# Optimization experiments

Measured on AMD Instinct MI355X. Metric: run time of the kernel, lower is better.

## Reference

```python
import jax, jax.numpy as jnp
import numpy as np

N_NODES = 50000
N_EDGES = 800000
IN_DIM = 256
HID = 256
NUM_LAYERS = 2


def _sage(xin, src, dst, inv_deg, W_l, b_l, W_r):
    # PyG SAGEConv (mean aggr): lin_l(mean of src features scattered to dst) + lin_r(x)
    agg = jax.ops.segment_sum(xin[src], dst, num_segments=xin.shape[0]) * inv_deg
    return agg @ W_l + b_l + xin @ W_r


def _mgdsgu(x, src, dst, inv_deg, h, Wx_l, bx_l, Wx_r, Wh_l, bh_l, Wh_r, Wb1, bb1, Wb2, bb2):
    # hid->hid conv order: 0=sage_hidden, 1=sage_single_h, 2=sage_update_h, 3=sage_candidate_h
    # in ->hid conv order: 0=sage_single_x, 1=sage_update_x, 2=sage_candidate_x
    h_N = _sage(h, src, dst, inv_deg, Wh_l[0], bh_l[0], Wh_r[0])
    # predict_missing_info: r = zeros so r_v = beta; gamma is computed in the
    # original but multiplied by zero -> no effect (omitted).
    beta = jnp.tanh(h @ Wb1 + bb1 + h_N @ Wb2 + bb2)
    m = h + beta - h_N
    h_N = h_N + m  # == h + beta, kept as written for clarity
    r = jax.nn.sigmoid(_sage(x, src, dst, inv_deg, Wx_l[0], bx_l[0], Wx_r[0])
                       + _sage(h_N, src, dst, inv_deg, Wh_l[1], bh_l[1], Wh_r[1]))
    z = jax.nn.sigmoid(_sage(x, src, dst, inv_deg, Wx_l[1], bx_l[1], Wx_r[1])
                       + _sage(h_N, src, dst, inv_deg, Wh_l[2], bh_l[2], Wh_r[2]))
    h_tilde = jnp.tanh(_sage(x, src, dst, inv_deg, Wx_l[2], bx_l[2], Wx_r[2])
                       + _sage(r * h_N, src, dst, inv_deg, Wh_l[3], bh_l[3], Wh_r[3]))
    return (1.0 - z) * h_N + z * h_tilde


def setup_inputs() -> dict:
    key = jax.random.key(0)
    ks = jax.random.split(key, 12)
    sx = 1.0 / np.sqrt(IN_DIM)
    sh = 1.0 / np.sqrt(HID)
    inp = {
        "x": jax.random.normal(ks[0], (N_NODES, IN_DIM), dtype=jnp.float32),
        "edge_index": jax.random.randint(ks[1], (2, N_EDGES), 0, N_NODES, dtype=jnp.int64),
        "Wx_l": jax.random.normal(ks[2], (3, IN_DIM, HID), dtype=jnp.float32) * sx,
        "bx_l": jnp.zeros((3, HID), dtype=jnp.float32),
        "Wx_r": jax.random.normal(ks[3], (3, IN_DIM, HID), dtype=jnp.float32) * sx,
        "Wh_l": jax.random.normal(ks[4], (4, HID, HID), dtype=jnp.float32) * sh,
        "bh_l": jnp.zeros((4, HID), dtype=jnp.float32),
        "Wh_r": jax.random.normal(ks[5], (4, HID, HID), dtype=jnp.float32) * sh,
        "Wb1": jax.random.normal(ks[6], (HID, HID), dtype=jnp.float32) * sh,
        "bb1": jnp.zeros((HID,), dtype=jnp.float32),
        "Wb2": jax.random.normal(ks[7], (HID, HID), dtype=jnp.float32) * sh,
        "bb2": jnp.zeros((HID,), dtype=jnp.float32),
        "We1": jax.random.normal(ks[8], (2 * HID, HID), dtype=jnp.float32) * (1.0 / np.sqrt(2 * HID)),
        "be1": jnp.zeros((HID,), dtype=jnp.float32),
        "We2": jax.random.normal(ks[9], (HID, 1), dtype=jnp.float32) * sh,
        "be2": jnp.zeros((1,), dtype=jnp.float32),
    }
    return inp


def reference(x, edge_index, Wx_l, bx_l, Wx_r, Wh_l, bh_l, Wh_r,
              Wb1, bb1, Wb2, bb2, We1, be1, We2, be2):
    src, dst = edge_index[0], edge_index[1]
    deg = jax.ops.segment_sum(jnp.ones((src.shape[0],), dtype=x.dtype), dst,
                              num_segments=x.shape[0])
    inv_deg = (1.0 / jnp.maximum(deg, 1.0))[:, None]  # [N, 1]

    h = jnp.zeros((x.shape[0], HID), dtype=x.dtype)
    for _ in range(NUM_LAYERS):
        h = _mgdsgu(x, src, dst, inv_deg, h, Wx_l, bx_l, Wx_r,
                    Wh_l, bh_l, Wh_r, Wb1, bb1, Wb2, bb2)

    # edge embeddings: concat(src emb, dst emb) -> MLP -> sigmoid
    edge_emb = jnp.concatenate([h[src], h[dst]], axis=1)  # [E, 2H]
    hidden = jax.nn.relu(edge_emb @ We1 + be1)
    preds = jax.nn.sigmoid(hidden @ We2 + be2)  # [E, 1]
    return (preds, h)
```

## Files before the change

kernel.cpp:

```cpp
#include <hip/hip_runtime.h>
#include <math.h>

#define HID 256
#define LROW 40

typedef __bf16 bf16x8 __attribute__((ext_vector_type(8)));
typedef float  f32x4  __attribute__((ext_vector_type(4)));
typedef unsigned short us8 __attribute__((ext_vector_type(8)));

__device__ __forceinline__ float sigmoidf_(float x){ return 1.0f/(1.0f + __expf(-x)); }
__device__ __forceinline__ unsigned short f2b(float f){
  __bf16 b = (__bf16)f; return __builtin_bit_cast(unsigned short, b);
}
__device__ __forceinline__ float b2f(unsigned short u){
  return (float)__builtin_bit_cast(__bf16, u);
}

__device__ __forceinline__ int edge_src(const int* ei, int e, int is64){
  return is64 ? ei[2*e] : ei[e];
}
__device__ __forceinline__ int edge_dst(const int* ei, int e, int E, int is64){
  return is64 ? ei[2*(E+e)] : ei[E+e];
}

__global__ void detect_kernel(const int* __restrict__ ei, int* __restrict__ flag){
  __shared__ int any;
  if (threadIdx.x == 0) any = 0;
  __syncthreads();
  if (ei[2*threadIdx.x + 1] != 0) atomicOr(&any, 1);
  __syncthreads();
  if (threadIdx.x == 0) *flag = any ? 0 : 1;
}

__global__ void count_kernel(const int* __restrict__ ei, const int* __restrict__ flag,
                             int* __restrict__ deg_i, int E){
  int e = blockIdx.x*blockDim.x + threadIdx.x;
  if (e >= E) return;
  int is64 = *flag;
  atomicAdd(&deg_i[edge_dst(ei,e,E,is64)], 1);
}

__global__ __launch_bounds__(1024) void scan_kernel(const int* __restrict__ deg_i,
  int* __restrict__ row_ptr, float* __restrict__ inv_deg, int N)
{
  __shared__ int wsum[16];
  __shared__ int carry_s;
  int tid = threadIdx.x, lane = tid & 63, wid = tid >> 6;
  if (tid == 0) carry_s = 0;
  __syncthreads();
  for (int base = 0; base < N; base += 1024){
    int i = base + tid;
    int v = (i < N) ? deg_i[i] : 0;
    int s = v;
    #pragma unroll
    for (int off = 1; off < 64; off <<= 1){
      int t = __shfl_up(s, off, 64);
      if (lane >= off) s += t;
    }
    if (lane == 63) wsum[wid] = s;
    __syncthreads();
    if (tid == 0){
      int run = 0;
      for (int w2 = 0; w2 < 16; ++w2){ int t = wsum[w2]; wsum[w2] = run; run += t; }
    }
    __syncthreads();
    int excl = carry_s + wsum[wid] + s - v;
    if (i < N){
      row_ptr[i] = excl;
      inv_deg[i] = 1.0f / fmaxf((float)v, 1.0f);
    }
    __syncthreads();
    if (tid == 1023) carry_s = excl + v;
    __syncthreads();
  }
  if (threadIdx.x == 0) row_ptr[N] = carry_s;
}

__global__ void fill_kernel(const int* __restrict__ ei, const int* __restrict__ flag,
                            const int* __restrict__ row_ptr, int* __restrict__ cursor,
                            int* __restrict__ col_src, int E){
  int e = blockIdx.x*blockDim.x + threadIdx.x;
  if (e >= E) return;
  int is64 = *flag;
  int d = edge_dst(ei,e,E,is64);
  int pos = atomicAdd(&cursor[d], 1);
  col_src[row_ptr[d] + pos] = edge_src(ei,e,is64);
}

__global__ __launch_bounds__(256) void conv_kernel(const float* __restrict__ in,
                                                   unsigned short* __restrict__ out, int n4){
  int i = blockIdx.x*256 + threadIdx.x;
  if (i >= n4) return;
  float4 v = *(const float4*)&in[(size_t)i*4];
  ushort4 o; o.x=f2b(v.x); o.y=f2b(v.y); o.z=f2b(v.z); o.w=f2b(v.w);
  *(ushort4*)&out[(size_t)i*4] = o;
}

__global__ __launch_bounds__(256) void wconv_kernel(
  const float* __restrict__ Wx_l, const float* __restrict__ Wx_r,
  const float* __restrict__ Wh_l, const float* __restrict__ Wh_r,
  const float* __restrict__ Wb1,  const float* __restrict__ Wb2,
  const float* __restrict__ We1,  unsigned short* __restrict__ Wt)
{
  int widx = blockIdx.x;
  int n = blockIdx.y;
  int k = threadIdx.x;
  const float* src;
  if      (widx < 3)  src = Wx_l + widx*65536;
  else if (widx < 6)  src = Wx_r + (widx-3)*65536;
  else if (widx < 10) src = Wh_l + (widx-6)*65536;
  else if (widx < 14) src = Wh_r + (widx-10)*65536;
  else if (widx == 14) src = Wb1;
  else if (widx == 15) src = Wb2;
  else                src = We1 + (widx-16)*65536;
  Wt[(size_t)widx*65536 + n*256 + k] = f2b(src[k*256 + n]);
}

__global__ __launch_bounds__(256) void comp_kernel(
  const float* __restrict__ A, const float* __restrict__ B,
  const float* __restrict__ add, unsigned short* __restrict__ dst)
{
  __shared__ float col[256];
  int n = blockIdx.x, k = threadIdx.x;
  col[k] = B[k*256 + n];
  __syncthreads();
  float s = add ? add[k*256 + n] : 0.f;
  #pragma unroll 8
  for (int j = 0; j < 256; ++j) s = fmaf(A[k*256 + j], col[j], s);
  dst[n*256 + k] = f2b(s);
}

__global__ __launch_bounds__(256) void aggregate_b_kernel(
    const unsigned short* __restrict__ X, unsigned short* __restrict__ out,
    const int* __restrict__ row_ptr, const int* __restrict__ col_src,
    const float* __restrict__ inv_deg, int N)
{
  int v = blockIdx.x*4 + (threadIdx.x >> 6);
  int lane = threadIdx.x & 63;
  if (v >= N) return;
  int beg = row_ptr[v], end = row_ptr[v+1];
  float a0=0.f, a1=0.f, a2=0.f, a3=0.f;
  int e = beg;
  for (; e + 8 <= end; e += 8){
    int sidx[8];
    #pragma unroll
    for (int t = 0; t < 8; ++t) sidx[t] = col_src[e + t];
    #pragma unroll
    for (int t = 0; t < 8; ++t){
      ushort4 u = *(const ushort4*)&X[(size_t)sidx[t]*HID + lane*4];
      a0 += b2f(u.x); a1 += b2f(u.y); a2 += b2f(u.z); a3 += b2f(u.w);
    }
  }
  for (; e < end; ++e){
    int s0 = col_src[e];
    ushort4 u = *(const ushort4*)&X[(size_t)s0*HID + lane*4];
    a0 += b2f(u.x); a1 += b2f(u.y); a2 += b2f(u.z); a3 += b2f(u.w);
  }
  float w = inv_deg[v];
  ushort4 o; o.x=f2b(a0*w); o.y=f2b(a1*w); o.z=f2b(a2*w); o.w=f2b(a3*w);
  *(ushort4*)&out[(size_t)v*HID + lane*4] = o;
}

__global__ __launch_bounds__(256) void rowprep_kernel(
  const float* __restrict__ bh_l, const float* __restrict__ bb1, const float* __restrict__ bb2,
  const float* __restrict__ Wb2, const float* __restrict__ Wh_l, const float* __restrict__ Wh_r,
  float* __restrict__ brow, float* __restrict__ hrow,
  float* __restrict__ rowL1, float* __restrict__ rowR1,
  float* __restrict__ rowL2, float* __restrict__ rowR2)
{
  __shared__ float sh[256];
  __shared__ float sh2[256];
  int j = threadIdx.x;
  sh[j] = bh_l[j];
  __syncthreads();
  float acc = bb1[j] + bb2[j];
  for (int k = 0; k < 256; ++k) acc = fmaf(sh[k], Wb2[k*256 + j], acc);
  float hr = tanhf(acc);
  brow[j] = acc;
  hrow[j] = hr; sh2[j] = hr;
  __syncthreads();
  const float* Whl1 = Wh_l + 65536;  const float* Whr1 = Wh_r + 65536;
  const float* Whl2 = Wh_l + 131072; const float* Whr2 = Wh_r + 131072;
  float a1=0.f, b1=0.f, a2=0.f, b2v=0.f;
  for (int k = 0; k < 256; ++k){
    float hv = sh2[k];
    a1  = fmaf(hv, Whl1[k*256+j], a1);
    b1  = fmaf(hv, Whr1[k*256+j], b1);
    a2  = fmaf(hv, Whl2[k*256+j], a2);
    b2v = fmaf(hv, Whr2[k*256+j], b2v);
  }
  rowL1[j] = a1; rowR1[j] = b1 + bh_l[256 + j];
  rowL2[j] = a2; rowR2[j] = b2v + bh_l[512 + j];
}

struct GJob {
  const unsigned short *A0,*W0,*A1,*W1,*A2,*W2,*A3,*W3;
  const float *bias,*bias2,*Z,*HN;
  const float *rowA,*rowB,*mulrow,*mulmat;
  const int* deg;
  float* outF; unsigned short* outB;
  int hn_bcast;
};

template<int MODE>
__global__ __launch_bounds__(512) void mgemm3_kernel(GJob j0, GJob j1, int M)
{
  __shared__ unsigned short Al[128*LROW];
  __shared__ unsigned short Wl[256*LROW];
  const GJob& J = blockIdx.y ? j1 : j0;
  const int tid  = threadIdx.x;
  const int lane = tid & 63, w = tid >> 6;
  const int wr = w >> 2, wc = w & 3;
  const int lane15 = lane & 15, laneq = (lane >> 4) * 8;
  const int row0 = blockIdx.x * 128;

  f32x4 acc[4][4];
  #pragma unroll
  for (int m = 0; m < 4; ++m)
    #pragma unroll
    for (int n = 0; n < 4; ++n) acc[m][n] = (f32x4)0.f;

  const unsigned short* pa[4]; const unsigned short* pw[4];
  int np = 0;
  if (J.A0){ pa[np]=J.A0; pw[np]=J.W0; ++np; }
  if (J.A1){ pa[np]=J.A1; pw[np]=J.W1; ++np; }
  if (J.A2){ pa[np]=J.A2; pw[np]=J.W2; ++np; }
  if (J.A3){ pa[np]=J.A3; pw[np]=J.W3; ++np; }
  const int steps = np * 8;

  const int strow = tid >> 2;
  const int koff  = (tid & 3) * 8;
  const int garow = (row0 + strow > M-1) ? (M-1) : (row0 + strow);
  const size_t abase  = (size_t)garow*HID + koff;
  const size_t wbase0 = (size_t)strow*HID + koff;
  const size_t wbase1 = (size_t)(strow + 128)*HID + koff;
  const int asidx  = strow*LROW + koff;
  const int wsidx0 = strow*LROW + koff;
  const int wsidx1 = (strow + 128)*LROW + koff;

  uint4 Ar0,Wr0a,Wr0b, Ar1,Wr1a,Wr1b;
  auto loadR = [&](int sp, uint4& a, uint4& wa, uint4& wb){
    const unsigned short* Ap = pa[sp >> 3];
    const unsigned short* Wp = pw[sp >> 3];
    const int k0 = (sp & 7) * 32;
    a  = *(const uint4*)(Ap + abase  + k0);
    wa = *(const uint4*)(Wp + wbase0 + k0);
    wb = *(const uint4*)(Wp + wbase1 + k0);
  };
  auto compute = [&](){
    bf16x8 af[4], bfr[4];
    #pragma unroll
    for (int m = 0; m < 4; ++m)
      af[m] = *(const bf16x8*)&Al[(wr*64 + m*16 + lane15)*LROW + laneq];
    #pragma unroll
    for (int n = 0; n < 4; ++n)
      bfr[n] = *(const bf16x8*)&Wl[(wc*64 + n*16 + lane15)*LROW + laneq];
    #pragma unroll
    for (int m = 0; m < 4; ++m)
      #pragma unroll
      for (int n = 0; n < 4; ++n)
        acc[m][n] = __builtin_amdgcn_mfma_f32_16x16x32_bf16(af[m], bfr[n], acc[m][n], 0, 0, 0);
  };

  loadR(0, Ar0,Wr0a,Wr0b);
  loadR(1, Ar1,Wr1a,Wr1b);
  for (int s = 0; s < steps; s += 2){
    __syncthreads();
    *(uint4*)&Al[asidx]  = Ar0;
    *(uint4*)&Wl[wsidx0] = Wr0a;
    *(uint4*)&Wl[wsidx1] = Wr0b;
    __syncthreads();
    if (s + 2 < steps) loadR(s+2, Ar0,Wr0a,Wr0b);
    compute();
    __syncthreads();
    *(uint4*)&Al[asidx]  = Ar1;
    *(uint4*)&Wl[wsidx0] = Wr1a;
    *(uint4*)&Wl[wsidx1] = Wr1b;
    __syncthreads();
    if (s + 3 < steps) loadR(s+3, Ar1,Wr1a,Wr1b);
    compute();
  }

  #pragma unroll
  for (int n = 0; n < 4; ++n){
    int gc = wc*64 + n*16 + lane15;
    float badd = 0.f;
    if (J.bias)  badd += J.bias[gc];
    if (J.bias2) badd += J.bias2[gc];
    float rA = 0.f, rB = 0.f, mr = 1.f, hnb = 0.f;
    if (MODE == 1){
      if (J.rowA){ rA = J.rowA[gc]; rB = J.rowB[gc]; }
      if (J.mulrow) mr = J.mulrow[gc];
    }
    if (MODE == 3 && J.hn_bcast) hnb = J.HN[gc];
    #pragma unroll
    for (int m = 0; m < 4; ++m){
      int rbse = row0 + wr*64 + m*16 + ((lane >> 4) << 2);
      #pragma unroll
      for (int r = 0; r < 4; ++r){
        int gr = rbse + r;
        if (gr >= M) continue;
        size_t idx = (size_t)gr*HID + gc;
        float p = acc[m][n][r] + badd;
        float v;
        if (MODE == 0) v = p;
        else if (MODE == 1){
          float g = (J.rowA && J.deg) ? ((J.deg[gr] > 0) ? 1.f : 0.f) : 0.f;
          v = sigmoidf_(p + g*rA + rB);
          if (J.mulrow) v *= mr;
          if (J.mulmat) v *= J.mulmat[idx];
        } else if (MODE == 2){
          v = J.HN[idx] + tanhf(p);
        } else {
          float z  = J.Z[idx];
          float hv = J.hn_bcast ? hnb : J.HN[idx];
          v = (1.f - z)*hv + z*tanhf(p);
        }
        if (J.outF) J.outF[idx] = v;
        if (J.outB) J.outB[idx] = f2b(v);
      }
    }
  }
}

__global__ __launch_bounds__(256) void edge_pred_kernel(
  const unsigned short* __restrict__ P, const unsigned short* __restrict__ Q,
  const int* __restrict__ ei, const int* __restrict__ flag,
  const float* __restrict__ We2, const float* __restrict__ be2,
  float* __restrict__ preds, int E)
{
  int wid = blockIdx.x*8 + (threadIdx.x >> 5);
  int l = threadIdx.x & 31;
  if (wid >= E) return;
  int is64 = *flag;
  int s = edge_src(ei, wid, is64);
  int d = edge_dst(ei, wid, E, is64);
  us8 p8 = *(const us8*)&P[(size_t)s*HID + l*8];
  us8 q8 = *(const us8*)&Q[(size_t)d*HID + l*8];
  float4 w0 = *(const float4*)&We2[l*8];
  float4 w1 = *(const float4*)&We2[l*8 + 4];
  float part = 0.f;
  #pragma unroll
  for (int j = 0; j < 4; ++j)
    part = fmaf(fmaxf(b2f(p8[j]) + b2f(q8[j]), 0.f), (&w0.x)[j], part);
  #pragma unroll
  for (int j = 0; j < 4; ++j)
    part = fmaf(fmaxf(b2f(p8[4+j]) + b2f(q8[4+j]), 0.f), (&w1.x)[j], part);
  #pragma unroll
  for (int off = 16; off > 0; off >>= 1) part += __shfl_down(part, off, 32);
  if (l == 0) preds[wid] = sigmoidf_(part + be2[0]);
}

typedef const unsigned short* cus;
typedef const float* cf;

template<int MODE>
static void launch_f(const GJob& a, const GJob* b, int M, hipStream_t s){
  dim3 g((M + 127)/128, b ? 2 : 1), blk(512);
  mgemm3_kernel<MODE><<<g, blk, 0, s>>>(a, b ? *b : a, M);
}

extern "C" void kernel_launch(void* const* d_in, const int* in_sizes, int n_in,
                              void* d_out, int out_size, void* d_ws, size_t ws_size,
                              hipStream_t stream)
{
  const float* x    = (const float*)d_in[0];
  const int*   ei   = (const int*)  d_in[1];
  const float* Wx_l = (const float*)d_in[2];
  const float* bx_l = (const float*)d_in[3];
  const float* Wx_r = (const float*)d_in[4];
  const float* Wh_l = (const float*)d_in[5];
  const float* bh_l = (const float*)d_in[6];
  const float* Wh_r = (const float*)d_in[7];
  const float* Wb1  = (const float*)d_in[8];
  const float* bb1  = (const float*)d_in[9];
  const float* Wb2  = (const float*)d_in[10];
  const float* bb2  = (const float*)d_in[11];
  const float* We1  = (const float*)d_in[12];
  const float* be1  = (const float*)d_in[13];
  const float* We2  = (const float*)d_in[14];
  const float* be2  = (const float*)d_in[15];

  const int N = in_sizes[0] / HID;
  const int E = in_sizes[1] / 2;
  cf NUL = nullptr; cus NUB = nullptr; const int* NULI = nullptr;

  size_t off = 0;
  auto alloc = [&](size_t bytes) -> void* {
    void* p = (char*)d_ws + off;
    off += (bytes + 255) & ~(size_t)255;
    return p;
  };
  int*   deg_i   = (int*)  alloc((size_t)N*4);
  int*   cursor  = (int*)  alloc((size_t)N*4);
  int*   row_ptr = (int*)  alloc(((size_t)N+1)*4);
  int*   col_src = (int*)  alloc((size_t)E*4);
  float* inv_deg = (float*)alloc((size_t)N*4);
  int*   flag    = (int*)  alloc(256);
  float* brow    = (float*)alloc(1024);
  float* hrow    = (float*)alloc(1024);
  float* rowL1   = (float*)alloc(1024);
  float* rowR1   = (float*)alloc(1024);
  float* rowL2   = (float*)alloc(1024);
  float* rowR2   = (float*)alloc(1024);
  unsigned short* Wt = (unsigned short*)alloc((size_t)18*65536*2);
  float* F0 = (float*)alloc((size_t)N*HID*4);
  float* F1 = (float*)alloc((size_t)N*HID*4);
  unsigned short* b0 = (unsigned short*)alloc((size_t)N*HID*2);
  unsigned short* b1 = (unsigned short*)alloc((size_t)N*HID*2);
  unsigned short* b2 = (unsigned short*)alloc((size_t)N*HID*2);
  unsigned short* b3 = (unsigned short*)alloc((size_t)N*HID*2);
  unsigned short* b4 = (unsigned short*)alloc((size_t)N*HID*2);

  float* preds = (float*)d_out;
  float* H     = preds + E;

  auto WT = [&](int i) -> cus { return Wt + (size_t)i*65536; };
  const float* bx0 = bx_l;  const float* bx1 = bx_l + 256; const float* bx2 = bx_l + 512;
  const float* bh1 = bh_l + 256;
  const float* bh2 = bh_l + 512; const float* bh3 = bh_l + 768;

  const int eb  = (E + 255)/256;
  const int nb4 = (N + 3)/4;
  const int n4b = (N*64 + 255)/256;

  auto mkjob = [&](cus A0,cus W0,cus A1,cus W1,cus A2,cus W2,cus A3,cus W3,
                   cf bias, cf bias2, cf Z, cf HN, int hnb,
                   cf rA, cf rB, cf mr, cf mm, const int* dg,
                   float* oF, unsigned short* oB) -> GJob {
    GJob g;
    g.A0=A0; g.W0=W0; g.A1=A1; g.W1=W1; g.A2=A2; g.W2=W2; g.A3=A3; g.W3=W3;
    g.bias=bias; g.bias2=bias2; g.Z=Z; g.HN=HN; g.hn_bcast=hnb;
    g.rowA=rA; g.rowB=rB; g.mulrow=mr; g.mulmat=mm; g.deg=dg;
    g.outF=oF; g.outB=oB;
    return g;
  };

  hipMemsetAsync(deg_i, 0, (size_t)N*4, stream);
  hipMemsetAsync(cursor, 0, (size_t)N*4, stream);
  detect_kernel<<<1,256,0,stream>>>(ei, flag);
  count_kernel<<<eb,256,0,stream>>>(ei, flag, deg_i, E);
  scan_kernel<<<1,1024,0,stream>>>(deg_i, row_ptr, inv_deg, N);
  fill_kernel<<<eb,256,0,stream>>>(ei, flag, row_ptr, cursor, col_src, E);

  conv_kernel<<<n4b,256,0,stream>>>(x, b0, N*64);
  wconv_kernel<<<dim3(18,256),256,0,stream>>>(Wx_l, Wx_r, Wh_l, Wh_r, Wb1, Wb2, We1, Wt);
  comp_kernel<<<256,256,0,stream>>>(Wh_l, Wb2, nullptr, (unsigned short*)WT(14));
  comp_kernel<<<256,256,0,stream>>>(Wh_r, Wb2, Wb1,     (unsigned short*)WT(15));
  rowprep_kernel<<<1,256,0,stream>>>(bh_l, bb1, bb2, Wb2, Wh_l, Wh_r,
                                     brow, hrow, rowL1, rowR1, rowL2, rowR2);

  aggregate_b_kernel<<<nb4,256,0,stream>>>(b0, b1, row_ptr, col_src, inv_deg, N);
  {
    GJob jt = mkjob(b1,WT(0), b0,WT(3), NUB,NUB, NUB,NUB, bx0,NUL, NUL,NUL,0,
                    rowL1,rowR1, hrow,NUL, deg_i, nullptr, b2);
    GJob jz = mkjob(b1,WT(1), b0,WT(4), NUB,NUB, NUB,NUB, bx1,NUL, NUL,NUL,0,
                    rowL2,rowR2, NUL,NUL, deg_i, F0, nullptr);
    launch_f<1>(jt, &jz, N, stream);
  }
  aggregate_b_kernel<<<nb4,256,0,stream>>>(b2, b3, row_ptr, col_src, inv_deg, N);
  {
    GJob jh = mkjob(b3,WT(9), b2,WT(13), b1,WT(2), b0,WT(5), bx2,bh3, F0,hrow,1,
                    NUL,NUL, NUL,NUL, NULI, F0, b4);
    launch_f<3>(jh, nullptr, N, stream);
  }

  aggregate_b_kernel<<<nb4,256,0,stream>>>(b4, b2, row_ptr, col_src, inv_deg, N);
  {
    GJob jn = mkjob(b2,WT(14), b4,WT(15), NUB,NUB, NUB,NUB, brow,NUL, NUL,F0,0,
                    NUL,NUL, NUL,NUL, NULI, F1, b3);
    launch_f<2>(jn, nullptr, N, stream);
  }
  aggregate_b_kernel<<<nb4,256,0,stream>>>(b3, b2, row_ptr, col_src, inv_deg, N);
  {
    GJob jt = mkjob(b2,WT(7), b3,WT(11), b1,WT(0), b0,WT(3), bx0,bh1, NUL,NUL,0,
                    NUL,NUL, NUL,F1, NULI, nullptr, b4);
    GJob jz = mkjob(b2,WT(8), b3,WT(12), b1,WT(1), b0,WT(4), bx1,bh2, NUL,NUL,0,
                    NUL,NUL, NUL,NUL, NULI, F0, nullptr);
    launch_f<1>(jt, &jz, N, stream);
  }
  aggregate_b_kernel<<<nb4,256,0,stream>>>(b4, b2, row_ptr, col_src, inv_deg, N);
  {
    GJob jh = mkjob(b2,WT(9), b4,WT(13), b1,WT(2), b0,WT(5), bx2,bh3, F0,F1,0,
                    NUL,NUL, NUL,NUL, NULI, H, b3);
    launch_f<3>(jh, nullptr, N, stream);
  }

  {
    GJob jp = mkjob(b3,WT(16), NUB,NUB, NUB,NUB, NUB,NUB, be1,NUL, NUL,NUL,0,
                    NUL,NUL, NUL,NUL, NULI, nullptr, b2);
    GJob jq = mkjob(b3,WT(17), NUB,NUB, NUB,NUB, NUB,NUB, NUL,NUL, NUL,NUL,0,
                    NUL,NUL, NUL,NUL, NULI, nullptr, b4);
    launch_f<0>(jp, &jq, N, stream);
  }
  edge_pred_kernel<<<(E+7)/8,256,0,stream>>>(b2, b4, ei, flag, We2, be2, preds, E);
}
```

Measured before the change: 1.160 ms.

## Precompute shared x-projections once and reuse across both GRU layers

The x-side SAGE projections (x and aggregated x against the three input weight sets) are identical in both layers. They are now computed once in a single three-job GEMM launch, stored as bf16/fp32 tensors, and added as epilogue inputs in later GEMMs, which cuts the K dimension of the layer-2 and candidate GEMMs from four operand pairs to two. Layer-1 gating moves to a separate elementwise kernel, and the GEMM tile is halved to 64 rows to give more blocks. The cost is extra intermediate traffic and bf16 rounding of the stored projections, which adds some precision risk.

Result: slower. 1.207 ms (+4.0%).

```diff
diff --git a/kernel.cpp b/kernel.cpp
--- a/kernel.cpp
+++ b/kernel.cpp
@@ -193,30 +193,61 @@
   rowL2[j] = a2; rowR2[j] = b2v + bh_l[512 + j];
 }
 
+__global__ __launch_bounds__(256) void l1_elem_kernel(
+  const unsigned short* __restrict__ xc0, const unsigned short* __restrict__ xc1,
+  const int* __restrict__ deg_i, const float* __restrict__ hrow,
+  const float* __restrict__ rowL1, const float* __restrict__ rowR1,
+  const float* __restrict__ rowL2, const float* __restrict__ rowR2,
+  unsigned short* __restrict__ t1, float* __restrict__ z1, int N)
+{
+  int idx = blockIdx.x*256 + threadIdx.x;
+  if (idx >= N*64) return;
+  int v = idx >> 6, j4 = (idx & 63) * 4;
+  float g = deg_i[v] > 0 ? 1.f : 0.f;
+  ushort4 a = *(const ushort4*)&xc0[(size_t)idx*4];
+  ushort4 b = *(const ushort4*)&xc1[(size_t)idx*4];
+  float4 L1 = *(const float4*)&rowL1[j4];
+  float4 R1 = *(const float4*)&rowR1[j4];
+  float4 L2 = *(const float4*)&rowL2[j4];
+  float4 R2 = *(const float4*)&rowR2[j4];
+  float4 hr = *(const float4*)&hrow[j4];
+  ushort4 t; float4 z;
+  t.x = f2b(sigmoidf_(b2f(a.x) + g*L1.x + R1.x) * hr.x);
+  t.y = f2b(sigmoidf_(b2f(a.y) + g*L1.y + R1.y) * hr.y);
+  t.z = f2b(sigmoidf_(b2f(a.z) + g*L1.z + R1.z) * hr.z);
+  t.w = f2b(sigmoidf_(b2f(a.w) + g*L1.w + R1.w) * hr.w);
+  z.x = sigmoidf_(b2f(b.x) + g*L2.x + R2.x);
+  z.y = sigmoidf_(b2f(b.y) + g*L2.y + R2.y);
+  z.z = sigmoidf_(b2f(b.z) + g*L2.z + R2.z);
+  z.w = sigmoidf_(b2f(b.w) + g*L2.w + R2.w);
+  *(ushort4*)&t1[(size_t)idx*4] = t;
+  *(float4*)&z1[(size_t)idx*4] = z;
+}
+
 struct GJob {
   const unsigned short *A0,*W0,*A1,*W1,*A2,*W2,*A3,*W3;
   const float *bias,*bias2,*Z,*HN;
-  const float *rowA,*rowB,*mulrow,*mulmat;
-  const int* deg;
+  const float *mulmat,*Df;
+  const unsigned short *Db,*Zb;
   float* outF; unsigned short* outB;
   int hn_bcast;
 };
 
 template<int MODE>
-__global__ __launch_bounds__(512) void mgemm3_kernel(GJob j0, GJob j1, int M)
-{
-  __shared__ unsigned short Al[128*LROW];
+__global__ __launch_bounds__(512) void mgemm4_kernel(GJob j0, GJob j1, GJob j2, int M)
+{
+  __shared__ unsigned short Al[64*LROW];
   __shared__ unsigned short Wl[256*LROW];
-  const GJob& J = blockIdx.y ? j1 : j0;
+  const GJob& J = (blockIdx.y == 0) ? j0 : ((blockIdx.y == 1) ? j1 : j2);
   const int tid  = threadIdx.x;
   const int lane = tid & 63, w = tid >> 6;
   const int wr = w >> 2, wc = w & 3;
   const int lane15 = lane & 15, laneq = (lane >> 4) * 8;
-  const int row0 = blockIdx.x * 128;
-
-  f32x4 acc[4][4];
+  const int row0 = blockIdx.x * 64;
+
+  f32x4 acc[2][4];
   #pragma unroll
-  for (int m = 0; m < 4; ++m)
+  for (int m = 0; m < 2; ++m)
     #pragma unroll
     for (int n = 0; n < 4; ++n) acc[m][n] = (f32x4)0.f;
 
@@ -228,35 +259,35 @@
   if (J.A3){ pa[np]=J.A3; pw[np]=J.W3; ++np; }
   const int steps = np * 8;
 
-  const int strow = tid >> 2;
-  const int koff  = (tid & 3) * 8;
-  const int garow = (row0 + strow > M-1) ? (M-1) : (row0 + strow);
-  const size_t abase  = (size_t)garow*HID + koff;
-  const size_t wbase0 = (size_t)strow*HID + koff;
-  const size_t wbase1 = (size_t)(strow + 128)*HID + koff;
-  const int asidx  = strow*LROW + koff;
-  const int wsidx0 = strow*LROW + koff;
-  const int wsidx1 = (strow + 128)*LROW + koff;
-
-  uint4 Ar0,Wr0a,Wr0b, Ar1,Wr1a,Wr1b;
-  auto loadR = [&](int sp, uint4& a, uint4& wa, uint4& wb){
+  const int arow  = tid >> 3;
+  const int akoff = (tid & 7) * 4;
+  const int garow = (row0 + arow > M-1) ? (M-1) : (row0 + arow);
+  const size_t abase = (size_t)garow*HID + akoff;
+  const int asidx = arow*LROW + akoff;
+  const int wrow  = tid >> 1;
+  const int wkoff = (tid & 1) * 16;
+  const size_t wbase = (size_t)wrow*HID + wkoff;
+  const int wsidx = wrow*LROW + wkoff;
+
+  uint2 Ar0, Ar1; uint4 Wr0a, Wr0b, Wr1a, Wr1b;
+  auto loadR = [&](int sp, uint2& a, uint4& wa, uint4& wb){
     const unsigned short* Ap = pa[sp >> 3];
     const unsigned short* Wp = pw[sp >> 3];
     const int k0 = (sp & 7) * 32;
-    a  = *(const uint4*)(Ap + abase  + k0);
-    wa = *(const uint4*)(Wp + wbase0 + k0);
-    wb = *(const uint4*)(Wp + wbase1 + k0);
+    a  = *(const uint2*)(Ap + abase + k0);
+    wa = *(const uint4*)(Wp + wbase + k0);
+    wb = *(const uint4*)(Wp + wbase + k0 + 8);
   };
   auto compute = [&](){
-    bf16x8 af[4], bfr[4];
-    #pragma unroll
-    for (int m = 0; m < 4; ++m)
-      af[m] = *(const bf16x8*)&Al[(wr*64 + m*16 + lane15)*LROW + laneq];
+    bf16x8 af[2], bfr[4];
+    #pragma unroll
+    for (int m = 0; m < 2; ++m)
+      af[m] = *(const bf16x8*)&Al[(wr*32 + m*16 + lane15)*LROW + laneq];
     #pragma unroll
     for (int n = 0; n < 4; ++n)
       bfr[n] = *(const bf16x8*)&Wl[(wc*64 + n*16 + lane15)*LROW + laneq];
     #pragma unroll
-    for (int m = 0; m < 4; ++m)
+    for (int m = 0; m < 2; ++m)
       #pragma unroll
       for (int n = 0; n < 4; ++n)
         acc[m][n] = __builtin_amdgcn_mfma_f32_16x16x32_bf16(af[m], bfr[n], acc[m][n], 0, 0, 0);
@@ -266,16 +297,16 @@
   loadR(1, Ar1,Wr1a,Wr1b);
   for (int s = 0; s < steps; s += 2){
     __syncthreads();
-    *(uint4*)&Al[asidx]  = Ar0;
-    *(uint4*)&Wl[wsidx0] = Wr0a;
-    *(uint4*)&Wl[wsidx1] = Wr0b;
+    *(uint2*)&Al[asidx]    = Ar0;
+    *(uint4*)&Wl[wsidx]    = Wr0a;
+    *(uint4*)&Wl[wsidx+8]  = Wr0b;
     __syncthreads();
     if (s + 2 < steps) loadR(s+2, Ar0,Wr0a,Wr0b);
     compute();
     __syncthreads();
-    *(uint4*)&Al[asidx]  = Ar1;
-    *(uint4*)&Wl[wsidx0] = Wr1a;
-    *(uint4*)&Wl[wsidx1] = Wr1b;
+    *(uint2*)&Al[asidx]    = Ar1;
+    *(uint4*)&Wl[wsidx]    = Wr1a;
+    *(uint4*)&Wl[wsidx+8]  = Wr1b;
     __syncthreads();
     if (s + 3 < steps) loadR(s+3, Ar1,Wr1a,Wr1b);
     compute();
@@ -287,32 +318,28 @@
     float badd = 0.f;
     if (J.bias)  badd += J.bias[gc];
     if (J.bias2) badd += J.bias2[gc];
-    float rA = 0.f, rB = 0.f, mr = 1.f, hnb = 0.f;
-    if (MODE == 1){
-      if (J.rowA){ rA = J.rowA[gc]; rB = J.rowB[gc]; }
-      if (J.mulrow) mr = J.mulrow[gc];
-    }
+    float hnb = 0.f;
     if (MODE == 3 && J.hn_bcast) hnb = J.HN[gc];
     #pragma unroll
-    for (int m = 0; m < 4; ++m){
-      int rbse = row0 + wr*64 + m*16 + ((lane >> 4) << 2);
+    for (int m = 0; m < 2; ++m){
+      int rbse = row0 + wr*32 + m*16 + ((lane >> 4) << 2);
       #pragma unroll
       for (int r = 0; r < 4; ++r){
         int gr = rbse + r;
         if (gr >= M) continue;
         size_t idx = (size_t)gr*HID + gc;
         float p = acc[m][n][r] + badd;
+        if (J.Df) p += J.Df[idx];
+        if (J.Db) p += b2f(J.Db[idx]);
         float v;
         if (MODE == 0) v = p;
         else if (MODE == 1){
-          float g = (J.rowA && J.deg) ? ((J.deg[gr] > 0) ? 1.f : 0.f) : 0.f;
-          v = sigmoidf_(p + g*rA + rB);
-          if (J.mulrow) v *= mr;
+          v = sigmoidf_(p);
           if (J.mulmat) v *= J.mulmat[idx];
         } else if (MODE == 2){
           v = J.HN[idx] + tanhf(p);
         } else {
-          float z  = J.Z[idx];
+          float z  = J.Z ? J.Z[idx] : b2f(J.Zb[idx]);
           float hv = J.hn_bcast ? hnb : J.HN[idx];
           v = (1.f - z)*hv + z*tanhf(p);
         }
@@ -355,9 +382,9 @@
 typedef const float* cf;
 
 template<int MODE>
-static void launch_f(const GJob& a, const GJob* b, int M, hipStream_t s){
-  dim3 g((M + 127)/128, b ? 2 : 1), blk(512);
-  mgemm3_kernel<MODE><<<g, blk, 0, s>>>(a, b ? *b : a, M);
+static void launch_f(const GJob* j, int nj, int M, hipStream_t s){
+  dim3 g((M + 63)/64, nj), blk(512);
+  mgemm4_kernel<MODE><<<g, blk, 0, s>>>(j[0], nj > 1 ? j[1] : j[0], nj > 2 ? j[2] : j[0], M);
 }
 
 extern "C" void kernel_launch(void* const* d_in, const int* in_sizes, int n_in,
@@ -383,7 +410,7 @@
 
   const int N = in_sizes[0] / HID;
   const int E = in_sizes[1] / 2;
-  cf NUL = nullptr; cus NUB = nullptr; const int* NULI = nullptr;
+  cf NUL = nullptr; cus NUB = nullptr;
 
   size_t off = 0;
   auto alloc = [&](size_t bytes) -> void* {
@@ -410,7 +437,6 @@
   unsigned short* b1 = (unsigned short*)alloc((size_t)N*HID*2);
   unsigned short* b2 = (unsigned short*)alloc((size_t)N*HID*2);
   unsigned short* b3 = (unsigned short*)alloc((size_t)N*HID*2);
-  unsigned short* b4 = (unsigned short*)alloc((size_t)N*HID*2);
 
   float* preds = (float*)d_out;
   float* H     = preds + E;
@@ -424,14 +450,14 @@
   const int nb4 = (N + 3)/4;
   const int n4b = (N*64 + 255)/256;
 
-  auto mkjob = [&](cus A0,cus W0,cus A1,cus W1,cus A2,cus W2,cus A3,cus W3,
-                   cf bias, cf bias2, cf Z, cf HN, int hnb,
-                   cf rA, cf rB, cf mr, cf mm, const int* dg,
+  auto mkjob = [&](cus A0,cus W0,cus A1,cus W1,
+                   cf bias, cf Z, cf HN, int hnb,
+                   cf mulmat, cf Df, cus Db, cus Zb,
                    float* oF, unsigned short* oB) -> GJob {
     GJob g;
-    g.A0=A0; g.W0=W0; g.A1=A1; g.W1=W1; g.A2=A2; g.W2=W2; g.A3=A3; g.W3=W3;
-    g.bias=bias; g.bias2=bias2; g.Z=Z; g.HN=HN; g.hn_bcast=hnb;
-    g.rowA=rA; g.rowB=rB; g.mulrow=mr; g.mulmat=mm; g.deg=dg;
+    g.A0=A0; g.W0=W0; g.A1=A1; g.W1=W1; g.A2=NUB; g.W2=NUB; g.A3=NUB; g.W3=NUB;
+    g.bias=bias; g.bias2=NUL; g.Z=Z; g.HN=HN; g.hn_bcast=hnb;
+    g.mulmat=mulmat; g.Df=Df; g.Db=Db; g.Zb=Zb;
     g.outF=oF; g.outB=oB;
     return g;
   };
@@ -452,46 +478,47 @@
 
   aggregate_b_kernel<<<nb4,256,0,stream>>>(b0, b1, row_ptr, col_src, inv_deg, N);
   {
-    GJob jt = mkjob(b1,WT(0), b0,WT(3), NUB,NUB, NUB,NUB, bx0,NUL, NUL,NUL,0,
-                    rowL1,rowR1, hrow,NUL, deg_i, nullptr, b2);
-    GJob jz = mkjob(b1,WT(1), b0,WT(4), NUB,NUB, NUB,NUB, bx1,NUL, NUL,NUL,0,
-                    rowL2,rowR2, NUL,NUL, deg_i, F0, nullptr);
-    launch_f<1>(jt, &jz, N, stream);
-  }
-  aggregate_b_kernel<<<nb4,256,0,stream>>>(b2, b3, row_ptr, col_src, inv_deg, N);
+    GJob j[3] = {
+      mkjob(b1,WT(0), b0,WT(3), bx0, NUL,NUL,0, NUL,NUL,NUB,NUB, nullptr, b2),
+      mkjob(b1,WT(1), b0,WT(4), bx1, NUL,NUL,0, NUL,NUL,NUB,NUB, nullptr, b3),
+      mkjob(b1,WT(2), b0,WT(5), bx2, NUL,NUL,0, NUL,NUL,NUB,NUB, F0, nullptr)
+    };
+    launch_f<0>(j, 3, N, stream);
+  }
+
+  l1_elem_kernel<<<n4b,256,0,stream>>>(b2, b3, deg_i, hrow, rowL1, rowR1,
+                                       rowL2, rowR2, b0, F1, N);
+  aggregate_b_kernel<<<nb4,256,0,stream>>>(b0, b1, row_ptr, col_src, inv_deg, N);
   {
-    GJob jh = mkjob(b3,WT(9), b2,WT(13), b1,WT(2), b0,WT(5), bx2,bh3, F0,hrow,1,
-                    NUL,NUL, NUL,NUL, NULI, F0, b4);
-    launch_f<3>(jh, nullptr, N, stream);
-  }
-
-  aggregate_b_kernel<<<nb4,256,0,stream>>>(b4, b2, row_ptr, col_src, inv_deg, N);
+    GJob j = mkjob(b1,WT(9), b0,WT(13), bh3, F1,hrow,1, NUL,F0,NUB,NUB, F1, b0);
+    launch_f<3>(&j, 1, N, stream);
+  }
+
+  aggregate_b_kernel<<<nb4,256,0,stream>>>(b0, b1, row_ptr, col_src, inv_deg, N);
   {
-    GJob jn = mkjob(b2,WT(14), b4,WT(15), NUB,NUB, NUB,NUB, brow,NUL, NUL,F0,0,
-                    NUL,NUL, NUL,NUL, NULI, F1, b3);
-    launch_f<2>(jn, nullptr, N, stream);
-  }
-  aggregate_b_kernel<<<nb4,256,0,stream>>>(b3, b2, row_ptr, col_src, inv_deg, N);
+    GJob j = mkjob(b1,WT(14), b0,WT(15), brow, NUL,F1,0, NUL,NUL,NUB,NUB, F1, b0);
+    launch_f<2>(&j, 1, N, stream);
+  }
+  aggregate_b_kernel<<<nb4,256,0,stream>>>(b0, b1, row_ptr, col_src, inv_deg, N);
   {
-    GJob jt = mkjob(b2,WT(7), b3,WT(11), b1,WT(0), b0,WT(3), bx0,bh1, NUL,NUL,0,
-                    NUL,NUL, NUL,F1, NULI, nullptr, b4);
-    GJob jz = mkjob(b2,WT(8), b3,WT(12), b1,WT(1), b0,WT(4), bx1,bh2, NUL,NUL,0,
-                    NUL,NUL, NUL,NUL, NULI, F0, nullptr);
-    launch_f<1>(jt, &jz, N, stream);
-  }
-  aggregate_b_kernel<<<nb4,256,0,stream>>>(b4, b2, row_ptr, col_src, inv_deg, N);
+    GJob j[2] = {
+      mkjob(b1,WT(7), b0,WT(11), bh1, NUL,NUL,0, F1,NUL,b2,NUB, nullptr, b2),
+      mkjob(b1,WT(8), b0,WT(12), bh2, NUL,NUL,0, NUL,NUL,b3,NUB, nullptr, b3)
+    };
+    launch_f<1>(j, 2, N, stream);
+  }
+  aggregate_b_kernel<<<nb4,256,0,stream>>>(b2, b1, row_ptr, col_src, inv_deg, N);
   {
-    GJob jh = mkjob(b2,WT(9), b4,WT(13), b1,WT(2), b0,WT(5), bx2,bh3, F0,F1,0,
-                    NUL,NUL, NUL,NUL, NULI, H, b3);
-    launch_f<3>(jh, nullptr, N, stream);
+    GJob j = mkjob(b1,WT(9), b2,WT(13), bh3, NUL,F1,0, NUL,F0,NUB,b3, H, b0);
+    launch_f<3>(&j, 1, N, stream);
   }
 
   {
-    GJob jp = mkjob(b3,WT(16), NUB,NUB, NUB,NUB, NUB,NUB, be1,NUL, NUL,NUL,0,
-                    NUL,NUL, NUL,NUL, NULI, nullptr, b2);
-    GJob jq = mkjob(b3,WT(17), NUB,NUB, NUB,NUB, NUB,NUB, NUL,NUL, NUL,NUL,0,
-                    NUL,NUL, NUL,NUL, NULI, nullptr, b4);
-    launch_f<0>(jp, &jq, N, stream);
-  }
-  edge_pred_kernel<<<(E+7)/8,256,0,stream>>>(b2, b4, ei, flag, We2, be2, preds, E);
-}
+    GJob j[2] = {
+      mkjob(b0,WT(16), NUB,NUB, be1, NUL,NUL,0, NUL,NUL,NUB,NUB, nullptr, b2),
+      mkjob(b0,WT(17), NUB,NUB, NUL, NUL,NUL,0, NUL,NUL,NUB,NUB, nullptr, b3)
+    };
+    launch_f<0>(j, 2, N, stream);
+  }
+  edge_pred_kernel<<<(E+7)/8,256,0,stream>>>(b2, b3, ei, flag, We2, be2, preds, E);
+}
```
